# Optimization experiments

Hardware: AMD Instinct MI355X
Metric: run time of the kernel (lower is better)

Reference implementation:

```python
import jax, jax.numpy as jnp
import numpy as np
from math import comb

N_SEG = 100000      # number of Bezier segments
BEZ_ORDER = 3       # cubic Bezier -> 4 control points per segment
D = 3               # point dimension
BATCH, NPTS = 8, 1000000


def setup_inputs() -> dict:
    key = jax.random.key(0)
    k1, k2, k3 = jax.random.split(key, 3)
    # strictly ascending knot vector: cumsum of positive dx, starting at 0
    dx = jax.random.uniform(k1, (N_SEG,), dtype=jnp.float32, minval=0.5, maxval=1.5)
    x_knots = jnp.concatenate([jnp.zeros((1,), jnp.float32), jnp.cumsum(dx)])
    x_end = x_knots[-1]
    # eval points spread beyond [0, x_end) so the modulo wrap is exercised
    x_eval = jax.random.uniform(k2, (BATCH, NPTS), dtype=jnp.float32) * (2.0 * x_end) - 0.5 * x_end
    control_points = jax.random.normal(k3, (N_SEG, BEZ_ORDER + 1, D), dtype=jnp.float32)
    return {"x_knots": x_knots, "control_points": control_points, "x_eval": x_eval}


def _bernstein_basis(s, n):
    # s: [N] in [0,1] -> basis [N, n+1]; powers via cumprod (differentiable at s=0/1)
    binom = jnp.asarray([comb(n, k) for k in range(n + 1)], dtype=s.dtype)
    t = s[:, None]
    ones = jnp.ones_like(t)
    t_pow = jnp.cumprod(jnp.concatenate([ones, jnp.broadcast_to(t, (t.shape[0], n))], axis=1), axis=1)         # t^k
    u = 1.0 - t
    u_pow = jnp.cumprod(jnp.concatenate([ones, jnp.broadcast_to(u, (u.shape[0], n))], axis=1), axis=1)         # u^k
    return binom * t_pow * u_pow[:, ::-1]  # C(n,k) t^k (1-t)^(n-k)


def reference(x_knots, control_points, x_eval):
    n = control_points.shape[1] - 1
    d = control_points.shape[2]
    xstart = x_knots[:-1]                      # [n_seg]
    dx = x_knots[1:] - x_knots[:-1]            # [n_seg]
    # x_true = x_eval % xend  (Python modulo semantics, matches torch %)
    x_true = jnp.mod(x_eval.reshape(-1), x_knots[-1])        # [N]
    # bucket search: segment index such that xstart[i] <= x_true < xstart[i+1]
    idx = jnp.clip(jnp.searchsorted(xstart, x_true, side='right') - 1, 0, xstart.shape[0] - 1)
    s = (x_true - xstart[idx]) / dx[idx]                     # local param in [0,1)
    basis = _bernstein_basis(s, n)                           # [N, n+1]
    P = control_points[idx]                                  # gather: [N, n+1, d]
    vals = jnp.einsum('nk,nkd->nd', basis, P)                # [N, d]
    return vals.reshape(x_eval.shape + (d,)), idx.reshape(x_eval.shape)
```

## Files before the change

kernel.cpp:

```cpp
#include <hip/hip_runtime.h>
#include <hip/hip_fp16.h>
#include <math.h>

#define N_SEG 100000
#define LUT_BITS 18
#define LUT_SIZE (1 << LUT_BITS)
#define DELTA 0.03
#define PPT 4

using f32x4 = __attribute__((ext_vector_type(4))) float;
using u32x4 = __attribute__((ext_vector_type(4))) unsigned int;

#define LUT_OFF 0
#define REC_OFF (2 << 20)
#define WS_NEED (REC_OFF + (size_t)N_SEG * 32)

__device__ __forceinline__ unsigned packh(float lo, float hi) {
    unsigned a = (unsigned)__half_as_ushort(__float2half(lo));
    unsigned b = (unsigned)__half_as_ushort(__float2half(hi));
    return a | (b << 16);
}
__device__ __forceinline__ float h2f(unsigned w, int hi) {
    return __half2float(__ushort_as_half((unsigned short)(hi ? (w >> 16) : (w & 0xFFFFu))));
}

__device__ __forceinline__ float mod_reduce(float x, float xe) {
    float r = x;
    r = (x >= xe) ? (x - xe) : r;
    r = (x < 0.0f) ? (x + xe) : r;
    return r;
}

__global__ void __launch_bounds__(256)
build_lut_kernel(const float* __restrict__ xk, int2* __restrict__ lut8) {
    int j = blockIdx.x * blockDim.x + threadIdx.x;
    if (j >= LUT_SIZE) return;
    double Wd = (double)xk[N_SEG] / (double)LUT_SIZE;
    double t = (double)j * Wd - DELTA;
    int lo = 0, hi = N_SEG;
    while (lo < hi) {
        int mid = (lo + hi) >> 1;
        if ((double)xk[mid] <= t) lo = mid + 1; else hi = mid;
    }
    int base = lo - 1;
    base = base < 0 ? 0 : (base > N_SEG - 1 ? N_SEG - 1 : base);
    int2 e;
    e.x = base;
    e.y = (base + 1 <= N_SEG - 1) ? __float_as_int(xk[base + 1])
                                  : __float_as_int(__builtin_inff());
    lut8[j] = e;
}

__global__ void __launch_bounds__(256)
build_rec_kernel(const float* __restrict__ xk, const float* __restrict__ cp,
                 u32x4* __restrict__ rec) {
    int i = blockIdx.x * blockDim.x + threadIdx.x;
    if (i >= N_SEG) return;
    float x0 = xk[i];
    float x1 = xk[i + 1];
    const f32x4* p = reinterpret_cast<const f32x4*>(cp + (size_t)i * 12);
    f32x4 a0 = p[0], a1 = p[1], a2 = p[2];
    u32x4 w0 = { __float_as_uint(x0), __float_as_uint(x1),
                 packh(a0.x, a0.y), packh(a0.z, a0.w) };
    u32x4 w1 = { packh(a1.x, a1.y), packh(a1.z, a1.w),
                 packh(a2.x, a2.y), packh(a2.z, a2.w) };
    rec[2 * (size_t)i]     = w0;
    rec[2 * (size_t)i + 1] = w1;
}

__device__ __forceinline__ void blend_sel(float r, u32x4 A0, u32x4 A1,
                                          float* v) {
    float x0 = __uint_as_float(A0.x);
    float x1 = __uint_as_float(A0.y);
    float s  = (r - x0) / (x1 - x0);

    float u = 1.0f - s;
    float s2 = s * s, u2 = u * u;
    float b0 = u2 * u;
    float b1 = (3.0f * s) * u2;
    float b2 = (3.0f * s2) * u;
    float b3 = s2 * s;

    float c0 = h2f(A0.z, 0), c1  = h2f(A0.z, 1);
    float c2 = h2f(A0.w, 0), c3  = h2f(A0.w, 1);
    float c4 = h2f(A1.x, 0), c5  = h2f(A1.x, 1);
    float c6 = h2f(A1.y, 0), c7  = h2f(A1.y, 1);
    float c8 = h2f(A1.z, 0), c9  = h2f(A1.z, 1);
    float c10 = h2f(A1.w, 0), c11 = h2f(A1.w, 1);

    v[0] = b0 * c0 + b1 * c3 + b2 * c6 + b3 * c9;
    v[1] = b0 * c1 + b1 * c4 + b2 * c7 + b3 * c10;
    v[2] = b0 * c2 + b1 * c5 + b2 * c8 + b3 * c11;
}

__global__ void __launch_bounds__(256)
eval_kernel(const float* __restrict__ xk,
            const float* __restrict__ xev,
            float* __restrict__ out_vals,
            float* __restrict__ out_idx,
            const unsigned char* __restrict__ ws,
            int npts) {
    __shared__ u32x4 stage[4 * PPT * 2 * 64];
    unsigned char* stg = reinterpret_cast<unsigned char*>(stage);
    const int2* lut8 = reinterpret_cast<const int2*>(ws + LUT_OFF);
    const unsigned char* rec = ws + REC_OFF;

    int t = blockIdx.x * blockDim.x + threadIdx.x;
    int lane = threadIdx.x & 63;
    int wave = threadIdx.x >> 6;
    unsigned wbase = (unsigned)wave * (PPT * 2 * 1024);
    long i0 = (long)t * PPT;

    float xe = xk[N_SEG];
    float invW = (float)LUT_SIZE / xe;

    if (i0 + PPT - 1 < (long)npts) {
        f32x4 x4 = __builtin_nontemporal_load(reinterpret_cast<const f32x4*>(xev) + t);
        float r[PPT] = {x4.x, x4.y, x4.z, x4.w};

        int2 e[PPT];
        #pragma unroll
        for (int q = 0; q < PPT; ++q) {
            r[q] = mod_reduce(r[q], xe);
            int j = (int)(r[q] * invW);
            j = j < 0 ? 0 : (j > LUT_SIZE - 1 ? LUT_SIZE - 1 : j);
            e[q] = lut8[j];
        }
        __builtin_amdgcn_sched_barrier(0);

        int idx[PPT];
        #pragma unroll
        for (int q = 0; q < PPT; ++q) {
            idx[q] = e[q].x + ((__int_as_float(e[q].y) <= r[q]) ? 1 : 0);
            const unsigned char* w = rec + (size_t)idx[q] * 32;
            #pragma unroll
            for (int k = 0; k < 2; ++k) {
                __builtin_amdgcn_global_load_lds(
                    (const __attribute__((address_space(1))) void*)(w + 16 * k),
                    (__attribute__((address_space(3))) void*)(stg + wbase + (q * 2 + k) * 1024 + lane * 16),
                    16, 0, 0);
            }
        }
        asm volatile("s_waitcnt vmcnt(0)" ::: "memory");
        __builtin_amdgcn_sched_barrier(0);

        float vals[PPT * 3];
        float idxf[PPT];
        #pragma unroll
        for (int q = 0; q < PPT; ++q) {
            const u32x4* pl = reinterpret_cast<const u32x4*>(stg + wbase + q * 2048 + lane * 16);
            u32x4 A0 = pl[0];
            u32x4 A1 = pl[64];
            blend_sel(r[q], A0, A1, &vals[q * 3]);
            idxf[q] = (float)idx[q];
        }
        f32x4* ov = reinterpret_cast<f32x4*>(out_vals + (size_t)t * 12);
        #pragma unroll
        for (int q = 0; q < 3; ++q) {
            f32x4 o = {vals[4 * q], vals[4 * q + 1], vals[4 * q + 2], vals[4 * q + 3]};
            ov[q] = o;
        }
        f32x4 oi = {idxf[0], idxf[1], idxf[2], idxf[3]};
        reinterpret_cast<f32x4*>(out_idx)[t] = oi;
    } else {
        for (long i = i0; i < (long)npts && i < i0 + PPT; ++i) {
            float r = mod_reduce(xev[i], xe);
            int j = (int)(r * invW);
            j = j < 0 ? 0 : (j > LUT_SIZE - 1 ? LUT_SIZE - 1 : j);
            int2 e = lut8[j];
            int idx = e.x + ((__int_as_float(e.y) <= r) ? 1 : 0);
            const u32x4* w = reinterpret_cast<const u32x4*>(rec + (size_t)idx * 32);
            u32x4 A0 = w[0], A1 = w[1];
            float v[3];
            blend_sel(r, A0, A1, v);
            out_vals[(size_t)i * 3 + 0] = v[0];
            out_vals[(size_t)i * 3 + 1] = v[1];
            out_vals[(size_t)i * 3 + 2] = v[2];
            out_idx[i] = (float)idx;
        }
    }
}

__global__ void __launch_bounds__(256)
eval_kernel_bs(const float* __restrict__ xk,
               const float* __restrict__ cp,
               const float* __restrict__ xev,
               float* __restrict__ out_vals,
               float* __restrict__ out_idx,
               int npts) {
    int i = blockIdx.x * blockDim.x + threadIdx.x;
    if (i >= npts) return;
    float xe = xk[N_SEG];
    float r = mod_reduce(xev[i], xe);
    int lo = 0, hi = N_SEG;
    while (lo < hi) {
        int mid = (lo + hi) >> 1;
        if (xk[mid] <= r) lo = mid + 1; else hi = mid;
    }
    int idx = lo - 1;
    if (idx < 0) idx = 0;
    float x0 = xk[idx];
    float s = (r - x0) / (xk[idx + 1] - x0);
    float u = 1.0f - s;
    float s2 = s * s, u2 = u * u;
    float b0 = u2 * u, b1f = (3.0f * s) * u2, b2f = (3.0f * s2) * u, b3f = s2 * s;
    const f32x4* p = reinterpret_cast<const f32x4*>(cp + (size_t)idx * 12);
    f32x4 pA = p[0], pB = p[1], pC = p[2];
    out_vals[(size_t)i * 3 + 0] = b0 * pA.x + b1f * pA.w + b2f * pB.z + b3f * pC.y;
    out_vals[(size_t)i * 3 + 1] = b0 * pA.y + b1f * pB.x + b2f * pB.w + b3f * pC.z;
    out_vals[(size_t)i * 3 + 2] = b0 * pA.z + b1f * pB.y + b2f * pC.x + b3f * pC.w;
    out_idx[i] = (float)idx;
}

extern "C" void kernel_launch(void* const* d_in, const int* in_sizes, int n_in,
                              void* d_out, int out_size, void* d_ws, size_t ws_size,
                              hipStream_t stream) {
    const float* xk  = (const float*)d_in[0];
    const float* cp  = (const float*)d_in[1];
    const float* xev = (const float*)d_in[2];
    int npts = in_sizes[2];

    float* out_vals = (float*)d_out;
    float* out_idx  = out_vals + (size_t)npts * 3;

    if (ws_size >= WS_NEED) {
        unsigned char* ws = (unsigned char*)d_ws;
        int2*  lut8 = (int2*)(ws + LUT_OFF);
        u32x4* rec  = (u32x4*)(ws + REC_OFF);
        build_lut_kernel<<<(LUT_SIZE + 255) / 256, 256, 0, stream>>>(xk, lut8);
        build_rec_kernel<<<(N_SEG + 255) / 256, 256, 0, stream>>>(xk, cp, rec);
        long nthreads = ((long)npts + PPT - 1) / PPT;
        int nblocks = (int)((nthreads + 255) / 256);
        eval_kernel<<<nblocks, 256, 0, stream>>>(xk, xev, out_vals, out_idx, ws, npts);
    } else {
        int nblocks = (npts + 255) / 256;
        eval_kernel_bs<<<nblocks, 256, 0, stream>>>(xk, cp, xev, out_vals, out_idx, npts);
    }
}
```

Measured before the change: 161.0 us.

## Replace LDS-staged record gathers with register gathers and double points per thread

Doubles points per thread from 4 to 8 and drops the global_load_lds staging through shared memory. Record gathers now load straight into registers, pinned with inline asm so all loads issue before any use. A launch-bounds occupancy hint is added. The aim is more memory-level parallelism per thread and removing the LDS round trip and shared-memory footprint, at the cost of higher register pressure and fewer threads.

```diff
diff --git a/kernel.cpp b/kernel.cpp
--- a/kernel.cpp
+++ b/kernel.cpp
@@ -6,7 +6,7 @@
 #define LUT_BITS 18
 #define LUT_SIZE (1 << LUT_BITS)
 #define DELTA 0.03
-#define PPT 4
+#define PPT 8
 
 using f32x4 = __attribute__((ext_vector_type(4))) float;
 using u32x4 = __attribute__((ext_vector_type(4))) unsigned int;
@@ -14,6 +14,8 @@
 #define LUT_OFF 0
 #define REC_OFF (2 << 20)
 #define WS_NEED (REC_OFF + (size_t)N_SEG * 32)
+
+#define PIN(x) asm volatile("" :: "v"(x))
 
 __device__ __forceinline__ unsigned packh(float lo, float hi) {
     unsigned a = (unsigned)__half_as_ushort(__float2half(lo));
@@ -68,8 +70,7 @@
     rec[2 * (size_t)i + 1] = w1;
 }
 
-__device__ __forceinline__ void blend_sel(float r, u32x4 A0, u32x4 A1,
-                                          float* v) {
+__device__ __forceinline__ void blend_sel(float r, u32x4 A0, u32x4 A1, float* v) {
     float x0 = __uint_as_float(A0.x);
     float x1 = __uint_as_float(A0.y);
     float s  = (r - x0) / (x1 - x0);
@@ -93,83 +94,88 @@
     v[2] = b0 * c2 + b1 * c5 + b2 * c8 + b3 * c11;
 }
 
-__global__ void __launch_bounds__(256)
+__global__ void __launch_bounds__(256, 4)
 eval_kernel(const float* __restrict__ xk,
             const float* __restrict__ xev,
             float* __restrict__ out_vals,
             float* __restrict__ out_idx,
             const unsigned char* __restrict__ ws,
             int npts) {
-    __shared__ u32x4 stage[4 * PPT * 2 * 64];
-    unsigned char* stg = reinterpret_cast<unsigned char*>(stage);
-    const int2* lut8 = reinterpret_cast<const int2*>(ws + LUT_OFF);
-    const unsigned char* rec = ws + REC_OFF;
+    const unsigned long long* lutL =
+        reinterpret_cast<const unsigned long long*>(ws + LUT_OFF);
+    const u32x4* rec = reinterpret_cast<const u32x4*>(ws + REC_OFF);
 
     int t = blockIdx.x * blockDim.x + threadIdx.x;
-    int lane = threadIdx.x & 63;
-    int wave = threadIdx.x >> 6;
-    unsigned wbase = (unsigned)wave * (PPT * 2 * 1024);
     long i0 = (long)t * PPT;
 
     float xe = xk[N_SEG];
     float invW = (float)LUT_SIZE / xe;
 
     if (i0 + PPT - 1 < (long)npts) {
-        f32x4 x4 = __builtin_nontemporal_load(reinterpret_cast<const f32x4*>(xev) + t);
-        float r[PPT] = {x4.x, x4.y, x4.z, x4.w};
-
-        int2 e[PPT];
+        f32x4 xa = __builtin_nontemporal_load(reinterpret_cast<const f32x4*>(xev) + 2 * t);
+        f32x4 xb = __builtin_nontemporal_load(reinterpret_cast<const f32x4*>(xev) + 2 * t + 1);
+        float r[PPT] = {xa.x, xa.y, xa.z, xa.w, xb.x, xb.y, xb.z, xb.w};
+        const unsigned long long* lp[PPT];
         #pragma unroll
         for (int q = 0; q < PPT; ++q) {
             r[q] = mod_reduce(r[q], xe);
             int j = (int)(r[q] * invW);
             j = j < 0 ? 0 : (j > LUT_SIZE - 1 ? LUT_SIZE - 1 : j);
-            e[q] = lut8[j];
-        }
+            lp[q] = lutL + j;
+        }
+        unsigned long long ev[PPT];
+        #pragma unroll
+        for (int q = 0; q < PPT; ++q) ev[q] = *lp[q];
         __builtin_amdgcn_sched_barrier(0);
+        #pragma unroll
+        for (int q = 0; q < PPT; ++q) PIN(ev[q]);
 
         int idx[PPT];
-        #pragma unroll
-        for (int q = 0; q < PPT; ++q) {
-            idx[q] = e[q].x + ((__int_as_float(e[q].y) <= r[q]) ? 1 : 0);
-            const unsigned char* w = rec + (size_t)idx[q] * 32;
-            #pragma unroll
-            for (int k = 0; k < 2; ++k) {
-                __builtin_amdgcn_global_load_lds(
-                    (const __attribute__((address_space(1))) void*)(w + 16 * k),
-                    (__attribute__((address_space(3))) void*)(stg + wbase + (q * 2 + k) * 1024 + lane * 16),
-                    16, 0, 0);
-            }
-        }
-        asm volatile("s_waitcnt vmcnt(0)" ::: "memory");
+        u32x4 A0[PPT], A1[PPT];
+        #pragma unroll
+        for (int q = 0; q < PPT; ++q) {
+            int base = (int)(unsigned)(ev[q] & 0xFFFFFFFFu);
+            float sel = __uint_as_float((unsigned)(ev[q] >> 32));
+            idx[q] = base + ((sel <= r[q]) ? 1 : 0);
+        }
+        #pragma unroll
+        for (int q = 0; q < PPT; ++q) {
+            const u32x4* w = rec + 2 * (size_t)idx[q];
+            A0[q] = w[0];
+            A1[q] = w[1];
+        }
         __builtin_amdgcn_sched_barrier(0);
+        #pragma unroll
+        for (int q = 0; q < PPT; ++q) { PIN(A0[q].x); PIN(A0[q].y); PIN(A0[q].z); PIN(A0[q].w);
+                                        PIN(A1[q].x); PIN(A1[q].y); PIN(A1[q].z); PIN(A1[q].w); }
 
         float vals[PPT * 3];
         float idxf[PPT];
         #pragma unroll
         for (int q = 0; q < PPT; ++q) {
-            const u32x4* pl = reinterpret_cast<const u32x4*>(stg + wbase + q * 2048 + lane * 16);
-            u32x4 A0 = pl[0];
-            u32x4 A1 = pl[64];
-            blend_sel(r[q], A0, A1, &vals[q * 3]);
+            blend_sel(r[q], A0[q], A1[q], &vals[q * 3]);
             idxf[q] = (float)idx[q];
         }
-        f32x4* ov = reinterpret_cast<f32x4*>(out_vals + (size_t)t * 12);
-        #pragma unroll
-        for (int q = 0; q < 3; ++q) {
+        f32x4* ov = reinterpret_cast<f32x4*>(out_vals + (size_t)t * (PPT * 3));
+        #pragma unroll
+        for (int q = 0; q < PPT * 3 / 4; ++q) {
             f32x4 o = {vals[4 * q], vals[4 * q + 1], vals[4 * q + 2], vals[4 * q + 3]};
             ov[q] = o;
         }
-        f32x4 oi = {idxf[0], idxf[1], idxf[2], idxf[3]};
-        reinterpret_cast<f32x4*>(out_idx)[t] = oi;
+        f32x4 oi0 = {idxf[0], idxf[1], idxf[2], idxf[3]};
+        f32x4 oi1 = {idxf[4], idxf[5], idxf[6], idxf[7]};
+        reinterpret_cast<f32x4*>(out_idx)[2 * t]     = oi0;
+        reinterpret_cast<f32x4*>(out_idx)[2 * t + 1] = oi1;
     } else {
         for (long i = i0; i < (long)npts && i < i0 + PPT; ++i) {
             float r = mod_reduce(xev[i], xe);
             int j = (int)(r * invW);
             j = j < 0 ? 0 : (j > LUT_SIZE - 1 ? LUT_SIZE - 1 : j);
-            int2 e = lut8[j];
-            int idx = e.x + ((__int_as_float(e.y) <= r) ? 1 : 0);
-            const u32x4* w = reinterpret_cast<const u32x4*>(rec + (size_t)idx * 32);
+            unsigned long long ev = lutL[j];
+            int base = (int)(unsigned)(ev & 0xFFFFFFFFu);
+            float sel = __uint_as_float((unsigned)(ev >> 32));
+            int idx = base + ((sel <= r) ? 1 : 0);
+            const u32x4* w = rec + 2 * (size_t)idx;
             u32x4 A0 = w[0], A1 = w[1];
             float v[3];
             blend_sel(r, A0, A1, v);
```

New measurement: 145.0 us (median of 2 runs). 1.11x faster.
